# Performance work log

Measured on AMD Instinct MI355X. Metric: run time of the kernel, lower is better.

The kernel has to match this reference:

```python
import jax, jax.numpy as jnp
import numpy as np

EPS_ATTN = 1e-6
EPS_LN = 1e-5  # torch nn.LayerNorm default eps
NHEAD = 8
L, D, DFF, S, B = 4, 512, 1024, 4096, 8


def _layernorm(x, g, b):
    m = jnp.mean(x, axis=-1, keepdims=True)
    v = jnp.mean((x - m) ** 2, axis=-1, keepdims=True)
    return (x - m) * jax.lax.rsqrt(v + EPS_LN) * g + b


def _layer(src, Wq, bq, Wk, bk, Wv, bv, Wo, bo, g1, be1, W1, bf1, W2, bf2, g2, be2):
    # src: (S, B, D)
    s, b, d = src.shape
    dk = d // NHEAD
    Q = (src @ Wq + bq).reshape(s, b, NHEAD, dk)
    K = (src @ Wk + bk).reshape(s, b, NHEAD, dk)
    V = (src @ Wv + bv).reshape(s, b, NHEAD, dk)
    # ELU+1 feature-map linear attention, vectorized over heads
    phiQ = jax.nn.elu(Q) + 1.0
    phiK = jax.nn.elu(K) + 1.0
    context = jnp.einsum('sbhd,sbhe->bhde', phiK, V)          # (B,H,dk,dk)
    out = jnp.einsum('sbhd,bhde->sbhe', phiQ, context)        # (S,B,H,dk)
    denom = jnp.einsum('sbhd,bhd->sbh', phiQ, phiK.sum(0))    # (S,B,H)
    out = out / (denom[..., None] + EPS_ATTN)
    attn = out.reshape(s, b, d)  # concat heads (same order as torch cat)
    out = attn @ Wo + bo
    out = _layernorm(src + out, g1, be1)
    ffn = jax.nn.relu(out @ W1 + bf1) @ W2 + bf2
    return _layernorm(out + ffn, g2, be2)


def setup_inputs() -> dict:
    key = jax.random.key(0)
    ks = jax.random.split(key, 8)
    sc = 0.02
    inp = {
        'src': jax.random.normal(ks[0], (S, B, D), jnp.float32),
        'Wq': jax.random.normal(ks[1], (L, D, D), jnp.float32) * sc,
        'bq': jnp.zeros((L, D), jnp.float32),
        'Wk': jax.random.normal(ks[2], (L, D, D), jnp.float32) * sc,
        'bk': jnp.zeros((L, D), jnp.float32),
        'Wv': jax.random.normal(ks[3], (L, D, D), jnp.float32) * sc,
        'bv': jnp.zeros((L, D), jnp.float32),
        'Wo': jax.random.normal(ks[4], (L, D, D), jnp.float32) * sc,
        'bo': jnp.zeros((L, D), jnp.float32),
        'ln1_g': jnp.ones((L, D), jnp.float32),
        'ln1_b': jnp.zeros((L, D), jnp.float32),
        'W1': jax.random.normal(ks[5], (L, D, DFF), jnp.float32) * sc,
        'b1': jnp.zeros((L, DFF), jnp.float32),
        'W2': jax.random.normal(ks[6], (L, DFF, D), jnp.float32) * sc,
        'b2': jnp.zeros((L, D), jnp.float32),
        'ln2_g': jnp.ones((L, D), jnp.float32),
        'ln2_b': jnp.zeros((L, D), jnp.float32),
    }
    return inp


def reference(src, Wq, bq, Wk, bk, Wv, bv, Wo, bo, ln1_g, ln1_b, W1, b1, W2, b2, ln2_g, ln2_b):
    x = src
    for i in range(Wq.shape[0]):  # small fixed layer count
        x = _layer(x, Wq[i], bq[i], Wk[i], bk[i], Wv[i], bv[i], Wo[i], bo[i],
                   ln1_g[i], ln1_b[i], W1[i], b1[i], W2[i], b2[i], ln2_g[i], ln2_b[i])
    return x
```

## Files before the change

kernel.cpp:

```cpp
#include <hip/hip_runtime.h>
#include <hip/hip_bf16.h>
#include <cstdint>

typedef __attribute__((ext_vector_type(8))) short short8;
typedef __attribute__((ext_vector_type(4))) float f32x4;
typedef __attribute__((ext_vector_type(4))) unsigned short ushort4v;

#define DEV static __device__ __forceinline__

DEV float bf2f(unsigned short u) {
    union { unsigned int i; float f; } v; v.i = ((unsigned int)u) << 16; return v.f;
}
DEV unsigned short f2bf(float f) {
    union { float f; unsigned int i; } v; v.f = f;
    unsigned int x = v.i;
    unsigned int r = x + 0x7fffu + ((x >> 16) & 1u);
    return (unsigned short)(r >> 16);
}

template<int EPI, int NBY, int LDA, int KT>
__global__ __launch_bounds__(256) void gemm_kernel(
    const unsigned short* __restrict__ A,
    const unsigned short* __restrict__ Bt,
    const float* __restrict__ bias,
    unsigned short* __restrict__ out1, int ldc1,
    unsigned short* __restrict__ out2)
{
    __shared__ unsigned short lds[128 * 136];
    const int t  = threadIdx.x;
    const int w  = t >> 6, l = t & 63;
    const int wr = w >> 1, wc = w & 1;
    const int lr = l & 15, lg = l >> 4;
    const int bid = blockIdx.x;
    const int j8  = bid & 7, s = bid >> 3;
    const int bx  = j8 * 32 + s / NBY;
    const int by  = s % NBY;
    const long tM = (long)bx * 128;
    const long tN = (long)by * 128;

    f32x4 acc[4][4];
#pragma unroll
    for (int i = 0; i < 4; i++)
#pragma unroll
        for (int j = 0; j < 4; j++) acc[i][j] = f32x4{0.f, 0.f, 0.f, 0.f};

    const unsigned short* ga[4];
    const unsigned short* gb[4];
    unsigned int ldsa[4], ldsb[4];
#pragma unroll
    for (int j = 0; j < 4; j++) {
        int c = (w * 4 + j) * 64 + l;
        int row = c >> 3, sc = (c & 7) ^ (row & 7);
        ga[j] = A + (tM + row) * LDA + sc * 8;
        gb[j] = Bt + (tN + row) * (long)KT + sc * 8;
        ldsa[j] = (w * 4 + j) * 512;
        ldsb[j] = 8192 + (w * 4 + j) * 512;
    }

#pragma unroll
    for (int kt = 0; kt < KT; kt += 64) {
#pragma unroll
        for (int j = 0; j < 4; j++)
            __builtin_amdgcn_global_load_lds(
                (const __attribute__((address_space(1))) void*)(ga[j] + kt),
                (__attribute__((address_space(3))) void*)(lds + ldsa[j]), 16, 0, 0);
#pragma unroll
        for (int j = 0; j < 4; j++)
            __builtin_amdgcn_global_load_lds(
                (const __attribute__((address_space(1))) void*)(gb[j] + kt),
                (__attribute__((address_space(3))) void*)(lds + ldsb[j]), 16, 0, 0);
        __syncthreads();
#pragma unroll
        for (int kk = 0; kk < 2; kk++) {
            short8 af[4], bfv[4];
#pragma unroll
            for (int mi = 0; mi < 4; mi++) {
                int r  = wr * 64 + mi * 16 + lr;
                int kc = kk * 4 + lg;
                af[mi] = *(const short8*)&lds[r * 64 + ((kc ^ (r & 7)) << 3)];
            }
#pragma unroll
            for (int ni = 0; ni < 4; ni++) {
                int n  = wc * 64 + ni * 16 + lr;
                int kc = kk * 4 + lg;
                bfv[ni] = *(const short8*)&lds[8192 + n * 64 + ((kc ^ (n & 7)) << 3)];
            }
#pragma unroll
            for (int mi = 0; mi < 4; mi++)
#pragma unroll
                for (int ni = 0; ni < 4; ni++)
                    acc[mi][ni] = __builtin_amdgcn_mfma_f32_16x16x32_bf16(
                        af[mi], bfv[ni], acc[mi][ni], 0, 0, 0);
        }
        __syncthreads();
    }

    float bv[4];
#pragma unroll
    for (int ni = 0; ni < 4; ni++) bv[ni] = bias[tN + wc * 64 + ni * 16 + lr];
    const bool doElu = (EPI == 0) && (tN < 512 || tN >= 1024);

#pragma unroll
    for (int mi = 0; mi < 4; mi++)
#pragma unroll
        for (int ni = 0; ni < 4; ni++)
#pragma unroll
            for (int j = 0; j < 4; j++) {
                float v = acc[mi][ni][j] + bv[ni];
                if (EPI == 0) { if (doElu) v = (v > 0.f) ? (v + 1.f) : expf(v); }
                if (EPI == 2) v = fmaxf(v, 0.f);
                int r = wr * 64 + mi * 16 + lg * 4 + j;
                int c = wc * 64 + ni * 16 + lr;
                lds[r * 136 + c] = f2bf(v);
            }
    __syncthreads();
    const bool toQ = (NBY == 12) && (tN >= 1024);
    unsigned short* o = toQ ? out2 : out1;
    const long ldc   = toQ ? 512 : ldc1;
    const long cb    = toQ ? (tN - 1024) : tN;
#pragma unroll
    for (int i = 0; i < 8; i++) {
        int q = i * 256 + t;
        int r = q >> 4, cc = q & 15;
        short8 v8 = *(const short8*)&lds[r * 136 + cc * 8];
        *(short8*)&o[(tM + r) * ldc + cb + cc * 8] = v8;
    }
}

template<int RESBF, int WRITEOF, int KT>
__global__ __launch_bounds__(512) void gemm_ln_kernel(
    const unsigned short* __restrict__ A, int lda,
    const unsigned short* __restrict__ Bt,
    const float* __restrict__ bias,
    const void* __restrict__ resp,
    const float* __restrict__ g,
    const float* __restrict__ be,
    float* __restrict__ of,
    unsigned short* __restrict__ ob,
    int unused)
{
    __shared__ unsigned short sA[2][128 * 32];
    __shared__ unsigned short sB[2][512 * 32];
    float* redb  = (float*)&sA[0][0];
    float* statb = redb + 1024;
    unsigned short* bb16 = (unsigned short*)&sB[0][0];
    const int t = threadIdx.x, w = t >> 6, l = t & 63, lr = l & 15, lg = l >> 4;
    const int wr = w >> 2, wc = w & 3;
    const long tM = (long)blockIdx.x * 128;

    f32x4 acc[4][8];
#pragma unroll
    for (int i = 0; i < 4; i++)
#pragma unroll
        for (int j = 0; j < 8; j++) acc[i][j] = f32x4{0.f, 0.f, 0.f, 0.f};

    const unsigned short* gA;
    const unsigned short* gB[4];
    unsigned int la, lb[4];
    {
        int c = t, row = c >> 2, sc = (c & 3) ^ ((row >> 1) & 3);
        gA = A + (tM + row) * (long)lda + sc * 8;
        la = (w * 64) * 8;
    }
#pragma unroll
    for (int j = 0; j < 4; j++) {
        int c = j * 512 + t, row = c >> 2, sc = (c & 3) ^ ((row >> 1) & 3);
        gB[j] = Bt + (long)row * KT + sc * 8;
        lb[j] = (j * 512 + w * 64) * 8;
    }

    auto STAGE = [&](int buf, int kt) {
        __builtin_amdgcn_global_load_lds(
            (const __attribute__((address_space(1))) void*)(gA + kt),
            (__attribute__((address_space(3))) void*)(&sA[buf][la]), 16, 0, 0);
#pragma unroll
        for (int j = 0; j < 4; j++)
            __builtin_amdgcn_global_load_lds(
                (const __attribute__((address_space(1))) void*)(gB[j] + kt),
                (__attribute__((address_space(3))) void*)(&sB[buf][lb[j]]), 16, 0, 0);
    };

    auto COMPUTE = [&](int buf) {
        short8 av[4], bw[8];
#pragma unroll
        for (int mi = 0; mi < 4; mi++) {
            int r = wr * 64 + mi * 16 + lr;
            av[mi] = *(const short8*)&sA[buf][r * 32 + ((lg ^ ((r >> 1) & 3)) << 3)];
        }
#pragma unroll
        for (int ni = 0; ni < 8; ni++) {
            int n = wc * 128 + ni * 16 + lr;
            bw[ni] = *(const short8*)&sB[buf][n * 32 + ((lg ^ ((n >> 1) & 3)) << 3)];
        }
#pragma unroll
        for (int mi = 0; mi < 4; mi++)
#pragma unroll
            for (int ni = 0; ni < 8; ni++)
                acc[mi][ni] = __builtin_amdgcn_mfma_f32_16x16x32_bf16(
                    av[mi], bw[ni], acc[mi][ni], 0, 0, 0);
    };

    STAGE(0, 0);
    __syncthreads();
#pragma unroll
    for (int kt = 32; kt < KT; kt += 32) {
        const int cur = ((kt >> 5) & 1) ^ 1;
        STAGE(cur ^ 1, kt);
        COMPUTE(cur);
        __syncthreads();
    }
    COMPUTE(((KT >> 5) & 1) ^ 1);

    const float* resf = (const float*)resp;
    const unsigned short* resb = (const unsigned short*)resp;
    float gv[8], bev[8], bb[8];
#pragma unroll
    for (int ni = 0; ni < 8; ni++) {
        int col = wc * 128 + ni * 16 + lr;
        gv[ni] = g[col]; bev[ni] = be[col]; bb[ni] = bias[col];
    }
#pragma unroll
    for (int mi = 0; mi < 4; mi++)
#pragma unroll
        for (int jj = 0; jj < 4; jj++) {
            long row = tM + wr * 64 + mi * 16 + lg * 4 + jj;
#pragma unroll
            for (int ni = 0; ni < 8; ni++) {
                int col = wc * 128 + ni * 16 + lr;
                float rv = RESBF ? bf2f(resb[row * 512 + col]) : resf[row * 512 + col];
                acc[mi][ni][jj] += bb[ni] + rv;
            }
        }
    float s2[4][4], ss2[4][4];
#pragma unroll
    for (int mi = 0; mi < 4; mi++)
#pragma unroll
        for (int jj = 0; jj < 4; jj++) {
            float s = 0.f, ss = 0.f;
#pragma unroll
            for (int ni = 0; ni < 8; ni++) {
                float v = acc[mi][ni][jj];
                s += v; ss += v * v;
            }
#pragma unroll
            for (int off = 1; off < 16; off <<= 1) {
                s  += __shfl_xor(s, off);
                ss += __shfl_xor(ss, off);
            }
            s2[mi][jj] = s; ss2[mi][jj] = ss;
        }
    __syncthreads();
    if (lr == 0) {
#pragma unroll
        for (int mi = 0; mi < 4; mi++)
#pragma unroll
            for (int jj = 0; jj < 4; jj++) {
                int rb = wr * 64 + mi * 16 + lg * 4 + jj;
                redb[0 * 512 + wc * 128 + rb] = s2[mi][jj];
                redb[1 * 512 + wc * 128 + rb] = ss2[mi][jj];
            }
    }
    __syncthreads();
    if (t < 128) {
        float S  = redb[t] + redb[128 + t] + redb[256 + t] + redb[384 + t];
        float SS = redb[512 + t] + redb[640 + t] + redb[768 + t] + redb[896 + t];
        float mean = S * (1.0f / 512.0f);
        float var  = SS * (1.0f / 512.0f) - mean * mean;
        statb[t] = mean;
        statb[128 + t] = rsqrtf(fmaxf(var, 0.f) + 1e-5f);
    }
    __syncthreads();
#pragma unroll
    for (int h = 0; h < 2; h++) {
        if (wr == h) {
#pragma unroll
            for (int mi = 0; mi < 4; mi++)
#pragma unroll
                for (int jj = 0; jj < 4; jj++) {
                    int rb  = mi * 16 + lg * 4 + jj;
                    int rbg = h * 64 + rb;
                    long row = tM + rbg;
                    float mean = statb[rbg], rstd = statb[128 + rbg];
#pragma unroll
                    for (int ni = 0; ni < 8; ni++) {
                        int col = wc * 128 + ni * 16 + lr;
                        float y = (acc[mi][ni][jj] - mean) * rstd * gv[ni] + bev[ni];
                        if (WRITEOF) of[row * 512 + col] = y;
                        bb16[rb * 512 + (col ^ ((rb & 7) << 3))] = f2bf(y);
                    }
                }
        }
        __syncthreads();
#pragma unroll
        for (int i = 0; i < 8; i++) {
            int q = i * 512 + t;
            int r = q >> 6, cc = q & 63;
            short8 v8 = *(const short8*)&bb16[r * 512 + ((cc ^ (r & 7)) << 3)];
            *(short8*)&ob[(tM + h * 64 + r) * 512 + cc * 8] = v8;
        }
        __syncthreads();
    }
}

__global__ __launch_bounds__(256) void ctx_partial_kernel(
    const unsigned short* __restrict__ kv, float* __restrict__ part,
    float* __restrict__ part2)
{
    const int p = blockIdx.x, ch = blockIdx.y;
    const int b = p >> 3, h = p & 7;
    __shared__ float kb[64 * 68];
    __shared__ float vbuf[64 * 68];
    const int t = threadIdx.x;
    const int dq = t >> 4, eq = t & 15;
    f32x4 acc[4];
    f32x4 ks = {0.f, 0.f, 0.f, 0.f};
#pragma unroll
    for (int i = 0; i < 4; i++) acc[i] = f32x4{0.f, 0.f, 0.f, 0.f};

    for (int sub = 0; sub < 8; sub++) {
        int sbase = ch * 512 + sub * 64;
#pragma unroll
        for (int i = 0; i < 2; i++) {
            int idx = i * 256 + t;
            int row = idx >> 3, c8 = idx & 7;
            long ga = ((long)(sbase + row) * 8 + b) * 1024 + h * 64 + c8 * 8;
            short8 kvv = *(const short8*)&kv[ga];
            short8 vv  = *(const short8*)&kv[ga + 512];
#pragma unroll
            for (int j = 0; j < 8; j++) {
                kb[row * 68 + c8 * 8 + j]   = bf2f((unsigned short)kvv[j]);
                vbuf[row * 68 + c8 * 8 + j] = bf2f((unsigned short)vv[j]);
            }
        }
        __syncthreads();
        for (int s = 0; s < 64; s++) {
            f32x4 k4 = *(const f32x4*)&kb[s * 68 + dq * 4];
            f32x4 v4 = *(const f32x4*)&vbuf[s * 68 + eq * 4];
#pragma unroll
            for (int i = 0; i < 4; i++) acc[i] += k4[i] * v4;
            ks += k4;
        }
        __syncthreads();
    }
    float* o = part + (long)(p * 8 + ch) * 4096;
#pragma unroll
    for (int i = 0; i < 4; i++)
        *(f32x4*)&o[(dq * 4 + i) * 64 + eq * 4] = acc[i];
    if (eq == 0)
        *(f32x4*)&part2[(p * 8 + ch) * 64 + dq * 4] = ks;
}

__global__ __launch_bounds__(256) void ctx_reduce_kernel(
    const float* __restrict__ part, const float* __restrict__ part2,
    unsigned short* __restrict__ ctxA)
{
    int o = (blockIdx.x * 256 + threadIdx.x) * 4;
    int p = o >> 12, d = (o >> 6) & 63, e0 = o & 63;
    f32x4 s = {0.f, 0.f, 0.f, 0.f};
    for (int ch = 0; ch < 8; ch++)
        s += *(const f32x4*)&part[(long)(p * 8 + ch) * 4096 + d * 64 + e0];
#pragma unroll
    for (int j = 0; j < 4; j++) ctxA[p * 5120 + (e0 + j) * 64 + d] = f2bf(s[j]);
    if (e0 == 0) {
        float ksv = 0.f;
#pragma unroll
        for (int ch = 0; ch < 8; ch++) ksv += part2[(p * 8 + ch) * 64 + d];
        ctxA[p * 5120 + 4096 + d] = f2bf(ksv);
#pragma unroll
        for (int j = 1; j < 16; j++) ctxA[p * 5120 + 4096 + j * 64 + d] = 0;
    }
}

__global__ __launch_bounds__(256) void attn_out_kernel(
    unsigned short* __restrict__ kv,
    const unsigned short* __restrict__ qbuf,
    const unsigned short* __restrict__ ctxA)
{
    __shared__ unsigned short abuf[256 * 68];
    const int p = blockIdx.x;
    const int b = p >> 3, h = p & 7;
    const int t = threadIdx.x, w = t >> 6, l = t & 63, lr = l & 15, lg = l >> 4;
    const int s0 = blockIdx.y * 256 + w * 64;
    f32x4 acc[4][5];
#pragma unroll
    for (int i = 0; i < 4; i++)
#pragma unroll
        for (int j = 0; j < 5; j++) acc[i][j] = f32x4{0.f, 0.f, 0.f, 0.f};
    const unsigned short* cb = ctxA + p * 5120;
#pragma unroll
    for (int kk = 0; kk < 2; kk++) {
        short8 af[4], bfv[5];
#pragma unroll
        for (int mi = 0; mi < 4; mi++) {
            int s = s0 + mi * 16 + lr;
            af[mi] = *(const short8*)&qbuf[((long)s * 8 + b) * 512 + h * 64 + kk * 32 + lg * 8];
        }
#pragma unroll
        for (int ni = 0; ni < 5; ni++)
            bfv[ni] = *(const short8*)&cb[(ni * 16 + lr) * 64 + kk * 32 + lg * 8];
#pragma unroll
        for (int mi = 0; mi < 4; mi++)
#pragma unroll
            for (int ni = 0; ni < 5; ni++)
                acc[mi][ni] = __builtin_amdgcn_mfma_f32_16x16x32_bf16(
                    af[mi], bfv[ni], acc[mi][ni], 0, 0, 0);
    }
#pragma unroll
    for (int mi = 0; mi < 4; mi++) {
#pragma unroll
        for (int j = 0; j < 4; j++) {
            float den = __shfl(acc[mi][4][j], (l & 48));
            float rc  = 1.0f / (den + 1e-6f);
            int rloc = w * 64 + mi * 16 + lg * 4 + j;
#pragma unroll
            for (int ni = 0; ni < 4; ni++)
                abuf[rloc * 68 + ni * 16 + lr] = f2bf(acc[mi][ni][j] * rc);
        }
    }
    __syncthreads();
    const int by256 = blockIdx.y * 256;
#pragma unroll
    for (int i = 0; i < 8; i++) {
        int q = i * 256 + t;
        int r = q >> 3, c8 = q & 7;
        short8 v8 = *(const short8*)&abuf[r * 68 + c8 * 8];
        long base = ((long)(by256 + r) * 8 + b) * 1024 + h * 64;
        *(short8*)&kv[base + c8 * 8] = v8;
    }
}

__global__ __launch_bounds__(256) void cvtbf_kernel(
    const float* __restrict__ x, unsigned short* __restrict__ y)
{
    long i = ((long)blockIdx.x * 256 + threadIdx.x) * 8;
    f32x4 a = *(const f32x4*)&x[i];
    f32x4 c = *(const f32x4*)&x[i + 4];
    short8 pk;
#pragma unroll
    for (int j = 0; j < 4; j++) { pk[j] = (short)f2bf(a[j]); pk[4 + j] = (short)f2bf(c[j]); }
    *(short8*)&y[i] = pk;
}

__global__ __launch_bounds__(256) void bcat_kernel(
    const float* __restrict__ bk, const float* __restrict__ bv,
    const float* __restrict__ bq, float* __restrict__ dst)
{
    int lyr = blockIdx.x;
    int j = blockIdx.y * 256 + threadIdx.x;
    float v;
    if (j < 512)       v = bk[lyr * 512 + j];
    else if (j < 1024) v = bv[lyr * 512 + j - 512];
    else               v = bq[lyr * 512 + j - 1024];
    dst[lyr * 1536 + j] = v;
}

__global__ __launch_bounds__(256) void wconv_kernel(
    const float* __restrict__ W, unsigned short* __restrict__ Wt, int K, int N,
    long lstrW, long lstrT)
{
    __shared__ float tile[64 * 65];
    const long lz = blockIdx.z;
    const float* Wl = W + lz * lstrW;
    unsigned short* Wtl = Wt + lz * lstrT;
    const int k0 = blockIdx.x * 64, n0 = blockIdx.y * 64;
    const int t = threadIdx.x;
#pragma unroll
    for (int i = 0; i < 4; i++) {
        int q = i * 256 + t;
        int r = q >> 4, c4 = q & 15;
        f32x4 v = *(const f32x4*)&Wl[(long)(k0 + r) * N + n0 + c4 * 4];
#pragma unroll
        for (int j = 0; j < 4; j++) tile[r * 65 + c4 * 4 + j] = v[j];
    }
    __syncthreads();
#pragma unroll
    for (int i = 0; i < 4; i++) {
        int q = i * 256 + t;
        int nr = q >> 4, kc = q & 15;
        ushort4v pk;
#pragma unroll
        for (int j = 0; j < 4; j++) pk[j] = f2bf(tile[(kc * 4 + j) * 65 + nr]);
        *(ushort4v*)&Wtl[(long)(n0 + nr) * K + k0 + kc * 4] = pk;
    }
}

extern "C" void kernel_launch(void* const* d_in, const int* in_sizes, int n_in,
                              void* d_out, int out_size, void* d_ws, size_t ws_size,
                              hipStream_t stream)
{
    const float* src  = (const float*)d_in[0];
    const float* Wq   = (const float*)d_in[1];
    const float* bq   = (const float*)d_in[2];
    const float* Wk   = (const float*)d_in[3];
    const float* bk   = (const float*)d_in[4];
    const float* Wv   = (const float*)d_in[5];
    const float* bv   = (const float*)d_in[6];
    const float* Wo   = (const float*)d_in[7];
    const float* bo   = (const float*)d_in[8];
    const float* l1g  = (const float*)d_in[9];
    const float* l1b  = (const float*)d_in[10];
    const float* W1   = (const float*)d_in[11];
    const float* b1   = (const float*)d_in[12];
    const float* W2   = (const float*)d_in[13];
    const float* b2   = (const float*)d_in[14];
    const float* l2g  = (const float*)d_in[15];
    const float* l2b  = (const float*)d_in[16];

    char* ws = (char*)d_ws;
    constexpr size_t SZ_WKVQ = (size_t)4 * 1536 * 512 * 2;
    constexpr size_t SZ_WO   = (size_t)4 * 512 * 512 * 2;
    constexpr size_t SZ_W1   = (size_t)4 * 512 * 1024 * 2;
    constexpr size_t SZ_W2   = SZ_W1;
    constexpr size_t SZ_BKVQ = (size_t)4 * 1536 * 4;
    constexpr size_t SZ_R1   = (size_t)32768 * 512 * 2;
    constexpr size_t SZ_KV   = (size_t)32768 * 1024 * 2;
    constexpr size_t OFF_WKVQ = 0;
    constexpr size_t OFF_WO   = OFF_WKVQ + SZ_WKVQ;
    constexpr size_t OFF_W1   = OFF_WO + SZ_WO;
    constexpr size_t OFF_W2   = OFF_W1 + SZ_W1;
    constexpr size_t OFF_BKVQ = OFF_W2 + SZ_W2;
    constexpr size_t OFF_R1   = OFF_BKVQ + SZ_BKVQ;
    constexpr size_t OFF_KV   = OFF_R1 + SZ_R1;
    constexpr size_t OFF_KSP  = OFF_KV + SZ_KV;
    constexpr size_t OFF_CTP  = OFF_KSP + (size_t)16 * 4096 * 4;
    constexpr size_t OFF_CTA  = OFF_CTP + (size_t)64 * 8 * 4096 * 4;

    unsigned short* WKVQ = (unsigned short*)(ws + OFF_WKVQ);
    unsigned short* WOT  = (unsigned short*)(ws + OFF_WO);
    unsigned short* W1T  = (unsigned short*)(ws + OFF_W1);
    unsigned short* W2T  = (unsigned short*)(ws + OFF_W2);
    float*          BKVQ = (float*)(ws + OFF_BKVQ);
    unsigned short* R1   = (unsigned short*)(ws + OFF_R1);
    unsigned short* KV   = (unsigned short*)(ws + OFF_KV);
    float*          KSP  = (float*)(ws + OFF_KSP);
    float*          CTP  = (float*)(ws + OFF_CTP);
    unsigned short* CTA  = (unsigned short*)(ws + OFF_CTA);
    float*          F1   = (float*)d_out;
    unsigned short* QBUF = (unsigned short*)d_out;

    dim3 blk(256);
    wconv_kernel<<<dim3(8, 8, 4),  blk, 0, stream>>>(Wk, WKVQ,             512, 512, 512*512, 1536*512);
    wconv_kernel<<<dim3(8, 8, 4),  blk, 0, stream>>>(Wv, WKVQ + 512*512,   512, 512, 512*512, 1536*512);
    wconv_kernel<<<dim3(8, 8, 4),  blk, 0, stream>>>(Wq, WKVQ + 1024*512,  512, 512, 512*512, 1536*512);
    wconv_kernel<<<dim3(8, 8, 4),  blk, 0, stream>>>(Wo, WOT,              512, 512, 512*512, 512*512);
    wconv_kernel<<<dim3(8, 16, 4), blk, 0, stream>>>(W1, W1T,              512, 1024, 512*1024, 512*1024);
    wconv_kernel<<<dim3(16, 8, 4), blk, 0, stream>>>(W2, W2T,              1024, 512, 1024*512, 1024*512);
    bcat_kernel<<<dim3(4, 6), blk, 0, stream>>>(bk, bv, bq, BKVQ);
    cvtbf_kernel<<<8192, blk, 0, stream>>>(src, R1);

    for (int lyr = 0; lyr < 4; lyr++) {
        const unsigned short* wkvq = WKVQ + (size_t)lyr * 1536 * 512;
        const unsigned short* wot  = WOT  + (size_t)lyr * 512 * 512;
        const unsigned short* w1t  = W1T  + (size_t)lyr * 512 * 1024;
        const unsigned short* w2t  = W2T  + (size_t)lyr * 1024 * 512;

        gemm_kernel<0, 12, 512, 512><<<3072, blk, 0, stream>>>(R1, wkvq, BKVQ + lyr * 1536,
                                                               KV, 1024, QBUF);

        ctx_partial_kernel<<<dim3(64, 8), blk, 0, stream>>>(KV, CTP, KSP);
        ctx_reduce_kernel<<<256, blk, 0, stream>>>(CTP, KSP, CTA);

        attn_out_kernel<<<dim3(64, 16), blk, 0, stream>>>(KV, QBUF, CTA);

        if (lyr == 0)
            gemm_ln_kernel<0, 0, 512><<<256, dim3(512), 0, stream>>>(KV, 1024, wot, bo + lyr * 512, src,
                                                                     l1g + lyr * 512, l1b + lyr * 512,
                                                                     F1, R1, 0);
        else
            gemm_ln_kernel<1, 0, 512><<<256, dim3(512), 0, stream>>>(KV, 1024, wot, bo + lyr * 512, R1,
                                                                     l1g + lyr * 512, l1b + lyr * 512,
                                                                     F1, R1, 0);
        gemm_kernel<2, 8, 512, 512><<<2048, blk, 0, stream>>>(R1, w1t, b1 + lyr * 1024,
                                                              KV, 1024, nullptr);
        if (lyr == 3)
            gemm_ln_kernel<1, 1, 1024><<<256, dim3(512), 0, stream>>>(KV, 1024, w2t, b2 + lyr * 512, R1,
                                                                      l2g + lyr * 512, l2b + lyr * 512,
                                                                      F1, R1, 0);
        else
            gemm_ln_kernel<1, 0, 1024><<<256, dim3(512), 0, stream>>>(KV, 1024, w2t, b2 + lyr * 512, R1,
                                                                      l2g + lyr * 512, l2b + lyr * 512,
                                                                      F1, R1, 0);
    }
}
```

Before: 1.128 ms.

## Double-buffer LDS with two-stage prefetch and manual vmcnt waits in GEMMs

Converts the plain GEMM kernel from a single-buffered load-sync-compute loop to a double-buffered pipeline that keeps two tiles in flight. The residual-LayerNorm GEMM gets the same two-ahead prefetch in place of its one-ahead scheme. Both use explicit s_waitcnt vmcnt counts and raw s_barrier instead of __syncthreads, so global-to-LDS loads overlap MFMA compute. This doubles LDS use, which may lower occupancy. The hard-coded vmcnt values must match the number of outstanding loads per stage.

```diff
diff --git a/kernel.cpp b/kernel.cpp
--- a/kernel.cpp
+++ b/kernel.cpp
@@ -26,7 +26,7 @@
     unsigned short* __restrict__ out1, int ldc1,
     unsigned short* __restrict__ out2)
 {
-    __shared__ unsigned short lds[128 * 136];
+    __shared__ unsigned short lds[32768];
     const int t  = threadIdx.x;
     const int w  = t >> 6, l = t & 63;
     const int wr = w >> 1, wc = w & 1;
@@ -46,30 +46,33 @@
 
     const unsigned short* ga[4];
     const unsigned short* gb[4];
-    unsigned int ldsa[4], ldsb[4];
+    unsigned int la[4], lb[4];
 #pragma unroll
     for (int j = 0; j < 4; j++) {
         int c = (w * 4 + j) * 64 + l;
         int row = c >> 3, sc = (c & 7) ^ (row & 7);
         ga[j] = A + (tM + row) * LDA + sc * 8;
         gb[j] = Bt + (tN + row) * (long)KT + sc * 8;
-        ldsa[j] = (w * 4 + j) * 512;
-        ldsb[j] = 8192 + (w * 4 + j) * 512;
-    }
-
-#pragma unroll
-    for (int kt = 0; kt < KT; kt += 64) {
+        la[j] = (w * 4 + j) * 512;
+        lb[j] = 8192 + (w * 4 + j) * 512;
+    }
+
+    auto STAGE = [&](int buf, int kt) {
+        const int base = buf * 16384;
 #pragma unroll
         for (int j = 0; j < 4; j++)
             __builtin_amdgcn_global_load_lds(
                 (const __attribute__((address_space(1))) void*)(ga[j] + kt),
-                (__attribute__((address_space(3))) void*)(lds + ldsa[j]), 16, 0, 0);
+                (__attribute__((address_space(3))) void*)(lds + base + la[j]), 16, 0, 0);
 #pragma unroll
         for (int j = 0; j < 4; j++)
             __builtin_amdgcn_global_load_lds(
                 (const __attribute__((address_space(1))) void*)(gb[j] + kt),
-                (__attribute__((address_space(3))) void*)(lds + ldsb[j]), 16, 0, 0);
-        __syncthreads();
+                (__attribute__((address_space(3))) void*)(lds + base + lb[j]), 16, 0, 0);
+    };
+
+    auto COMPUTE = [&](int buf) {
+        const int base = buf * 16384;
 #pragma unroll
         for (int kk = 0; kk < 2; kk++) {
             short8 af[4], bfv[4];
@@ -77,13 +80,13 @@
             for (int mi = 0; mi < 4; mi++) {
                 int r  = wr * 64 + mi * 16 + lr;
                 int kc = kk * 4 + lg;
-                af[mi] = *(const short8*)&lds[r * 64 + ((kc ^ (r & 7)) << 3)];
+                af[mi] = *(const short8*)&lds[base + r * 64 + ((kc ^ (r & 7)) << 3)];
             }
 #pragma unroll
             for (int ni = 0; ni < 4; ni++) {
                 int n  = wc * 64 + ni * 16 + lr;
                 int kc = kk * 4 + lg;
-                bfv[ni] = *(const short8*)&lds[8192 + n * 64 + ((kc ^ (n & 7)) << 3)];
+                bfv[ni] = *(const short8*)&lds[base + 8192 + n * 64 + ((kc ^ (n & 7)) << 3)];
             }
 #pragma unroll
             for (int mi = 0; mi < 4; mi++)
@@ -92,7 +95,19 @@
                     acc[mi][ni] = __builtin_amdgcn_mfma_f32_16x16x32_bf16(
                         af[mi], bfv[ni], acc[mi][ni], 0, 0, 0);
         }
-        __syncthreads();
+    };
+
+    STAGE(0, 0);
+    STAGE(1, 64);
+#pragma unroll
+    for (int kt = 0; kt < KT; kt += 64) {
+        if (kt < KT - 64) asm volatile("s_waitcnt vmcnt(8)" ::: "memory");
+        else              asm volatile("s_waitcnt vmcnt(0)" ::: "memory");
+        __builtin_amdgcn_s_barrier();
+        COMPUTE((kt >> 6) & 1);
+        asm volatile("s_waitcnt lgkmcnt(0)" ::: "memory");
+        __builtin_amdgcn_s_barrier();
+        if (kt + 128 < KT) STAGE((kt >> 6) & 1, kt + 128);
     }
 
     float bv[4];
@@ -201,15 +216,17 @@
     };
 
     STAGE(0, 0);
-    __syncthreads();
-#pragma unroll
-    for (int kt = 32; kt < KT; kt += 32) {
-        const int cur = ((kt >> 5) & 1) ^ 1;
-        STAGE(cur ^ 1, kt);
-        COMPUTE(cur);
-        __syncthreads();
-    }
-    COMPUTE(((KT >> 5) & 1) ^ 1);
+    STAGE(1, 32);
+#pragma unroll
+    for (int kt = 0; kt < KT; kt += 32) {
+        if (kt < KT - 32) asm volatile("s_waitcnt vmcnt(5)" ::: "memory");
+        else              asm volatile("s_waitcnt vmcnt(0)" ::: "memory");
+        __builtin_amdgcn_s_barrier();
+        COMPUTE((kt >> 5) & 1);
+        asm volatile("s_waitcnt lgkmcnt(0)" ::: "memory");
+        __builtin_amdgcn_s_barrier();
+        if (kt + 64 < KT) STAGE((kt >> 5) & 1, kt + 64);
+    }
 
     const float* resf = (const float*)resp;
     const unsigned short* resb = (const unsigned short*)resp;
```

After: 1.145 ms. No clear change (+1.5%).
